# Performance work log

Measured on AMD Instinct MI355X. Metric: run time of the kernel, lower is better.

## Reference

```python
import jax, jax.numpy as jnp
import numpy as np

NX, NQ, NU = 2048, 2048, 16
EPS = 0.01
STD = 0.5


def setup_inputs() -> dict:
    key = jax.random.key(0)
    ks = jax.random.split(key, 8)
    return {
        "t": 0,
        "x": jax.random.normal(ks[0], (NX,), dtype=jnp.float32),
        "u": jax.random.normal(ks[1], (NU,), dtype=jnp.float32),
        "X": jax.random.normal(ks[2], (NX + NQ, NX + NQ), dtype=jnp.float32) * STD,
        "U": jax.random.normal(ks[3], (NX, NQ), dtype=jnp.float32) * STD,
        "Y1": jax.random.normal(ks[4], (NX, NX), dtype=jnp.float32) * STD,
        "XP": jax.random.normal(ks[5], (NX, NX), dtype=jnp.float32) * STD,
        "B2": jax.random.normal(ks[6], (NX, NU), dtype=jnp.float32) * STD,
        "D12": jax.random.normal(ks[7], (NQ, NU), dtype=jnp.float32) * STD,
    }


def _constrained_mats(X, U, Y1, XP):
    nx = XP.shape[0]
    nq = U.shape[1]
    # P = XP XP^T + eps I ;  H = X X^T + eps I   (F.linear(A,B)=A@B.T)
    P = XP @ XP.T + EPS * jnp.eye(nx, dtype=XP.dtype)
    H = X @ X.T + EPS * jnp.eye(nx + nq, dtype=X.dtype)
    H11 = H[:nx, :nx]
    H12 = H[:nx, nx:]
    H22 = H[nx:, nx:]
    Y = -0.5 * (H11 + Y1 - Y1.T)
    Pinv = jnp.linalg.inv(P)
    A = Pinv @ Y                        # F.linear(inv(P), Y.T) = inv(P) @ Y
    lam = 0.5 * jnp.diagonal(H22)       # diagonal of Lambda
    D11 = -jnp.tril(H22, -1) / lam[:, None]   # strictly lower triangular
    C1 = U.T / lam[:, None]             # inv(Lambda) @ U.T
    B1 = Pinv @ (-H12 - U)
    return A, B1, C1, D11


def _solve_w(D11, c):
    nq = c.shape[0]

    def step(w, inp):
        i, d_row, ci = inp
        wi = jax.nn.relu(ci + jnp.dot(d_row, w))
        return w.at[i].set(wi), None

    w0 = jnp.zeros(nq, dtype=c.dtype)
    w, _ = jax.lax.scan(step, w0, (jnp.arange(nq), D11, c))
    return w


def reference(t, x, u, X, U, Y1, XP, B2, D12):
    A, B1, C1, D11 = _constrained_mats(X, U, Y1, XP)
    c = C1 @ x + D12 @ u                # precomputed affine part (bv = 0, bias=False)
    w = _solve_w(D11, c)
    x_dot = A @ x + B1 @ w + B2 @ u     # bx = 0
    return x_dot
```

## Files before the change

kernel.cpp:

```cpp
#include <hip/hip_runtime.h>
#include <math.h>

#define NQ2 2048
#define NT  4096
#define NUU 16
#define FEPS 0.01f
#define NB  64
#define NBLK 32
#define NSB 128
#define NSP 132
#define NSBLK 16
#define GCH 16

typedef __attribute__((ext_vector_type(8))) short short8;
typedef __attribute__((ext_vector_type(4))) float floatx4;

__device__ __forceinline__ float readlane_f(float v, int lane) {
  return __int_as_float(__builtin_amdgcn_readlane(__float_as_int(v), lane));
}

__device__ __forceinline__ unsigned short f2bf(float x) {
  unsigned u = __float_as_uint(x);
  unsigned r = u + 0x7FFFu + ((u >> 16) & 1u);
  return (unsigned short)(r >> 16);
}
__device__ __forceinline__ float bf2f(unsigned short h) {
  return __uint_as_float(((unsigned)h) << 16);
}

__device__ __forceinline__ float wave_reduce(float v) {
#pragma unroll
  for (int off = 32; off > 0; off >>= 1) v += __shfl_down(v, off, 64);
  return v;
}

__device__ __forceinline__ float block_reduce_256(float v) {
  __shared__ float sm[4];
  v = wave_reduce(v);
  if ((threadIdx.x & 63) == 0) sm[threadIdx.x >> 6] = v;
  __syncthreads();
  return (threadIdx.x == 0) ? (sm[0] + sm[1] + sm[2] + sm[3]) : 0.0f;
}

__global__ __launch_bounds__(256) void lam_kernel(const float* __restrict__ X,
                                                  float* __restrict__ invlam) {
  int row = blockIdx.x;
  const float* xr = X + (size_t)(NQ2 + row) * NT;
  float s = 0.f;
  for (int k = threadIdx.x * 4; k < NT; k += 1024) {
    float4 v = *(const float4*)(xr + k);
    s += v.x * v.x + v.y * v.y + v.z * v.z + v.w * v.w;
  }
  float tot = block_reduce_256(s);
  if (threadIdx.x == 0) invlam[row] = 1.0f / (0.5f * (tot + FEPS));
}

__global__ __launch_bounds__(256) void tgemv_part_kernel(const float* __restrict__ A,
                                                         const float* __restrict__ v,
                                                         float* __restrict__ part) {
  int col = blockIdx.x * 256 + threadIdx.x;
  int ch = blockIdx.y;
  int i0 = ch * (NQ2 / GCH), i1 = i0 + NQ2 / GCH;
  float s = 0.f;
#pragma unroll 4
  for (int i = i0; i < i1; i++) s = fmaf(A[(size_t)i * NQ2 + col], v[i], s);
  part[(size_t)ch * NQ2 + col] = s;
}

template <int FM>
__global__ __launch_bounds__(256) void finish_kernel(const float* __restrict__ part,
                                                     const float* __restrict__ invlam,
                                                     const float* __restrict__ D12,
                                                     const float* __restrict__ u,
                                                     float* __restrict__ dst) {
  int col = blockIdx.x * 256 + threadIdx.x;
  float s = 0.f;
#pragma unroll
  for (int ch = 0; ch < GCH; ch++) s += part[(size_t)ch * NQ2 + col];
  if (FM == 0) {
    float d = 0.f;
#pragma unroll
    for (int j = 0; j < NUU; j++) d += D12[(size_t)col * NUU + j] * u[j];
    dst[col] = s * invlam[col] + d;
  } else if (FM == 1) {
    dst[col] += 0.5f * s;
  } else {
    dst[col] = s;
  }
}

__global__ __launch_bounds__(256) void syrk_mfma_kernel(const float* __restrict__ A,
                                                        int lda, int K,
                                                        float* __restrict__ C, float eps) {
  int L = blockIdx.x;
  int bi = (int)((sqrtf(8.0f * (float)L + 1.0f) - 1.0f) * 0.5f);
  while ((bi + 1) * (bi + 2) / 2 <= L) bi++;
  while (bi * (bi + 1) / 2 > L) bi--;
  int bj = L - bi * (bi + 1) / 2;
  int row0 = bi * 128, col0 = bj * 128;

  __shared__ __align__(16) short Ah[4096], Al[4096], Bh[4096], Bl[4096];

  int tid = threadIdx.x;
  int l = tid & 63;
  int w = tid >> 6;
  int wr = w >> 1, wc = w & 1;

  int g0 = tid, g1 = tid + 256;
  int ar0 = (g0 >> 6) * 16 + (g0 & 15), ak0 = ((g0 >> 4) & 3) * 8;
  int ar1 = (g1 >> 6) * 16 + (g1 & 15), ak1 = ((g1 >> 4) & 3) * 8;

  const float* pa0 = A + (size_t)(row0 + ar0) * lda + ak0;
  const float* pa1 = A + (size_t)(row0 + ar1) * lda + ak1;
  const float* pb0 = A + (size_t)(col0 + ar0) * lda + ak0;
  const float* pb1 = A + (size_t)(col0 + ar1) * lda + ak1;

  floatx4 acc[4][4];
#pragma unroll
  for (int m = 0; m < 4; m++)
#pragma unroll
    for (int n = 0; n < 4; n++) acc[m][n] = (floatx4){0.f, 0.f, 0.f, 0.f};

  float xa0[8], xa1[8], xb0[8], xb1[8];
  {
    float4 t0 = *(const float4*)(pa0), t1 = *(const float4*)(pa0 + 4);
    xa0[0]=t0.x; xa0[1]=t0.y; xa0[2]=t0.z; xa0[3]=t0.w; xa0[4]=t1.x; xa0[5]=t1.y; xa0[6]=t1.z; xa0[7]=t1.w;
    t0 = *(const float4*)(pa1); t1 = *(const float4*)(pa1 + 4);
    xa1[0]=t0.x; xa1[1]=t0.y; xa1[2]=t0.z; xa1[3]=t0.w; xa1[4]=t1.x; xa1[5]=t1.y; xa1[6]=t1.z; xa1[7]=t1.w;
    t0 = *(const float4*)(pb0); t1 = *(const float4*)(pb0 + 4);
    xb0[0]=t0.x; xb0[1]=t0.y; xb0[2]=t0.z; xb0[3]=t0.w; xb0[4]=t1.x; xb0[5]=t1.y; xb0[6]=t1.z; xb0[7]=t1.w;
    t0 = *(const float4*)(pb1); t1 = *(const float4*)(pb1 + 4);
    xb1[0]=t0.x; xb1[1]=t0.y; xb1[2]=t0.z; xb1[3]=t0.w; xb1[4]=t1.x; xb1[5]=t1.y; xb1[6]=t1.z; xb1[7]=t1.w;
  }

  for (int k0 = 0; k0 < K; k0 += 32) {
    __syncthreads();
    {
      short8 h, lo;
#pragma unroll
      for (int j = 0; j < 8; j++) { unsigned short hb = f2bf(xa0[j]); h[j] = (short)hb; lo[j] = (short)f2bf(xa0[j] - bf2f(hb)); }
      *(short8*)&Ah[g0 * 8] = h; *(short8*)&Al[g0 * 8] = lo;
#pragma unroll
      for (int j = 0; j < 8; j++) { unsigned short hb = f2bf(xa1[j]); h[j] = (short)hb; lo[j] = (short)f2bf(xa1[j] - bf2f(hb)); }
      *(short8*)&Ah[g1 * 8] = h; *(short8*)&Al[g1 * 8] = lo;
#pragma unroll
      for (int j = 0; j < 8; j++) { unsigned short hb = f2bf(xb0[j]); h[j] = (short)hb; lo[j] = (short)f2bf(xb0[j] - bf2f(hb)); }
      *(short8*)&Bh[g0 * 8] = h; *(short8*)&Bl[g0 * 8] = lo;
#pragma unroll
      for (int j = 0; j < 8; j++) { unsigned short hb = f2bf(xb1[j]); h[j] = (short)hb; lo[j] = (short)f2bf(xb1[j] - bf2f(hb)); }
      *(short8*)&Bh[g1 * 8] = h; *(short8*)&Bl[g1 * 8] = lo;
    }
    __syncthreads();
    if (k0 + 32 < K) {
      const float* q = pa0 + k0 + 32;
      float4 t0 = *(const float4*)(q), t1 = *(const float4*)(q + 4);
      xa0[0]=t0.x; xa0[1]=t0.y; xa0[2]=t0.z; xa0[3]=t0.w; xa0[4]=t1.x; xa0[5]=t1.y; xa0[6]=t1.z; xa0[7]=t1.w;
      q = pa1 + k0 + 32; t0 = *(const float4*)(q); t1 = *(const float4*)(q + 4);
      xa1[0]=t0.x; xa1[1]=t0.y; xa1[2]=t0.z; xa1[3]=t0.w; xa1[4]=t1.x; xa1[5]=t1.y; xa1[6]=t1.z; xa1[7]=t1.w;
      q = pb0 + k0 + 32; t0 = *(const float4*)(q); t1 = *(const float4*)(q + 4);
      xb0[0]=t0.x; xb0[1]=t0.y; xb0[2]=t0.z; xb0[3]=t0.w; xb0[4]=t1.x; xb0[5]=t1.y; xb0[6]=t1.z; xb0[7]=t1.w;
      q = pb1 + k0 + 32; t0 = *(const float4*)(q); t1 = *(const float4*)(q + 4);
      xb1[0]=t0.x; xb1[1]=t0.y; xb1[2]=t0.z; xb1[3]=t0.w; xb1[4]=t1.x; xb1[5]=t1.y; xb1[6]=t1.z; xb1[7]=t1.w;
    }
    short8 amh[4], aml[4], bnh[4], bnl[4];
#pragma unroll
    for (int m = 0; m < 4; m++) {
      int ga = ((wr * 4 + m) * 64 + l) * 8;
      amh[m] = *(const short8*)&Ah[ga];
      aml[m] = *(const short8*)&Al[ga];
    }
#pragma unroll
    for (int n = 0; n < 4; n++) {
      int gb = ((wc * 4 + n) * 64 + l) * 8;
      bnh[n] = *(const short8*)&Bh[gb];
      bnl[n] = *(const short8*)&Bl[gb];
    }
#pragma unroll
    for (int m = 0; m < 4; m++)
#pragma unroll
      for (int n = 0; n < 4; n++) {
        acc[m][n] = __builtin_amdgcn_mfma_f32_16x16x32_bf16(amh[m], bnh[n], acc[m][n], 0, 0, 0);
        acc[m][n] = __builtin_amdgcn_mfma_f32_16x16x32_bf16(amh[m], bnl[n], acc[m][n], 0, 0, 0);
        acc[m][n] = __builtin_amdgcn_mfma_f32_16x16x32_bf16(aml[m], bnh[n], acc[m][n], 0, 0, 0);
      }
  }

  int lr = (l >> 4) * 4;
  int lc = l & 15;
#pragma unroll
  for (int m = 0; m < 4; m++)
#pragma unroll
    for (int n = 0; n < 4; n++)
#pragma unroll
      for (int r = 0; r < 4; r++) {
        int gi = row0 + wr * 64 + m * 16 + lr + r;
        int gj = col0 + wc * 64 + n * 16 + lc;
        float v = acc[m][n][r];
        if (gi == gj) v += eps;
        C[(size_t)gi * NQ2 + gj] = v;
      }
}

__global__ __launch_bounds__(512) void chol_diag128_kernel(float* __restrict__ M_,
                                                           float* __restrict__ Xinvs, int k) {
  __shared__ __align__(16) float Ls[NSB][NSP];
  __shared__ __align__(16) float Xs[NSB][NSP];
  __shared__ float Tmp[32][33];
  __shared__ float dinv[NSB];
  int b0 = k * NSB;
  int tid = threadIdx.x;
  int wv = tid >> 6;
  int lane = tid & 63;

  for (int e = tid; e < NSB * NSP; e += 512) ((float*)Xs)[e] = 0.f;
  for (int e = tid; e < NSB * NSB; e += 512) {
    int rr = e >> 7, cc = e & 127;
    Ls[rr][cc] = M_[(size_t)(b0 + rr) * NQ2 + b0 + cc];
  }
  __syncthreads();

#pragma unroll 1
  for (int kb = 0; kb < 4; kb++) {
    int o = kb * 32;
    if (wv == 0) {
      int r = lane & 31;
      float a[32];
#pragma unroll
      for (int j = 0; j < 32; j++) a[j] = Ls[o + r][o + j];
#pragma unroll
      for (int j = 0; j < 32; j++) {
        float d = readlane_f(a[j], j);
        float rs = rsqrtf(fmaxf(d, 1e-20f));
        a[j] *= rs;
        if (lane == 0) dinv[o + j] = rs;
#pragma unroll
        for (int k2 = j + 1; k2 < 32; k2++) {
          float ljk = readlane_f(a[j], k2);
          a[k2] = fmaf(-a[j], ljk, a[k2]);
        }
      }
      if (lane < 32) {
#pragma unroll
        for (int j = 0; j < 32; j++) Ls[o + r][o + j] = a[j];
      }
    }
    __syncthreads();
    int nrows = 96 - o;
    if (nrows > 0) {
      if (tid < nrows) {
        int r = o + 32 + tid;
        float v[32];
#pragma unroll
        for (int j = 0; j < 32; j++) v[j] = Ls[r][o + j];
#pragma unroll
        for (int t = 0; t < 32; t++) {
          v[t] *= dinv[o + t];
#pragma unroll
          for (int j = t + 1; j < 32; j++)
            v[j] = fmaf(-v[t], Ls[o + j][o + t], v[j]);
        }
#pragma unroll
        for (int j = 0; j < 32; j++) Ls[r][o + j] = v[j];
      }
      __syncthreads();
      int tot = nrows * nrows;
      for (int e = tid; e < tot; e += 512) {
        int rr = o + 32 + e / nrows, cc = o + 32 + e % nrows;
        float s = 0.f;
#pragma unroll
        for (int t = 0; t < 32; t += 4) {
          float4 a = *(const float4*)&Ls[rr][o + t];
          float4 b = *(const float4*)&Ls[cc][o + t];
          s += a.x * b.x + a.y * b.y + a.z * b.z + a.w * b.w;
        }
        Ls[rr][cc] -= s;
      }
      __syncthreads();
    }
  }

  if (wv < 4) {
    int o = wv * 32;
    int c = lane & 31;
    float x[32];
#pragma unroll
    for (int i = 0; i < 32; i++) x[i] = 0.f;
#pragma unroll
    for (int t = 0; t < 32; t++) {
      float rcpd = 1.0f / Ls[o + t][o + t];
      x[t] = (t == c) ? rcpd : x[t] * rcpd;
#pragma unroll
      for (int i = t + 1; i < 32; i++)
        x[i] = fmaf(-Ls[o + i][o + t], x[t], x[i]);
    }
    if (lane < 32) {
#pragma unroll
      for (int i = 0; i < 32; i++) Xs[o + i][o + c] = x[i];
    }
  }
  __syncthreads();

#pragma unroll 1
  for (int j = 0; j < 4; j++) {
#pragma unroll 1
    for (int i = j + 1; i < 4; i++) {
      int oi = i * 32, oj = j * 32;
      for (int e = tid; e < 32 * 32; e += 512) {
        int rr = e >> 5, cc = e & 31;
        float s = 0.f;
        for (int kk = j; kk < i; kk++) {
          int ok = kk * 32;
#pragma unroll
          for (int t = 0; t < 32; t += 4) {
            float4 a = *(const float4*)&Ls[oi + rr][ok + t];
            s += a.x * Xs[ok + t][oj + cc] + a.y * Xs[ok + t + 1][oj + cc]
               + a.z * Xs[ok + t + 2][oj + cc] + a.w * Xs[ok + t + 3][oj + cc];
          }
        }
        Tmp[rr][cc] = s;
      }
      __syncthreads();
      for (int e = tid; e < 32 * 32; e += 512) {
        int rr = e >> 5, cc = e & 31;
        float s = 0.f;
#pragma unroll
        for (int t = 0; t < 32; t += 4) {
          float4 a = *(const float4*)&Xs[oi + rr][oi + t];
          s += a.x * Tmp[t][cc] + a.y * Tmp[t + 1][cc]
             + a.z * Tmp[t + 2][cc] + a.w * Tmp[t + 3][cc];
        }
        Xs[oi + rr][oj + cc] = -s;
      }
      __syncthreads();
    }
  }

  float* Xp = Xinvs + (size_t)k * NSB * NSB;
  for (int e = tid; e < NSB * NSB; e += 512) {
    int rr = e >> 7, cc = e & 127;
    if (cc <= rr) M_[(size_t)(b0 + rr) * NQ2 + b0 + cc] = Ls[rr][cc];
    Xp[e] = Xs[rr][cc];
  }
}

__global__ __launch_bounds__(256) void chol_panel128_kernel(float* __restrict__ M_,
                                                            const float* __restrict__ Xinv,
                                                            int k) {
  int kc = k * NSB;
  int rb0 = kc + NSB + blockIdx.x * 128;
  __shared__ float As[16][128];
  __shared__ float Bs[16][128];
  int tid = threadIdx.x;
  int tx = tid & 15, ty = tid >> 4;
  int sr = tid >> 1, ks = (tid & 1) * 8;

  const float* ap = M_ + (size_t)(rb0 + sr) * NQ2 + kc + ks;
  const float* bp = Xinv + sr * 128 + ks;
  float4 a0 = *(const float4*)(ap), a1 = *(const float4*)(ap + 4);
  float4 b0 = *(const float4*)(bp), b1 = *(const float4*)(bp + 4);

  float acc[8][8] = {{0.f}};
  for (int k0 = 0; k0 < 128; k0 += 16) {
    __syncthreads();
    As[ks + 0][sr] = a0.x; As[ks + 1][sr] = a0.y; As[ks + 2][sr] = a0.z; As[ks + 3][sr] = a0.w;
    As[ks + 4][sr] = a1.x; As[ks + 5][sr] = a1.y; As[ks + 6][sr] = a1.z; As[ks + 7][sr] = a1.w;
    Bs[ks + 0][sr] = b0.x; Bs[ks + 1][sr] = b0.y; Bs[ks + 2][sr] = b0.z; Bs[ks + 3][sr] = b0.w;
    Bs[ks + 4][sr] = b1.x; Bs[ks + 5][sr] = b1.y; Bs[ks + 6][sr] = b1.z; Bs[ks + 7][sr] = b1.w;
    __syncthreads();
    if (k0 + 16 < 128) {
      const float* q = ap + k0 + 16;
      a0 = *(const float4*)(q); a1 = *(const float4*)(q + 4);
      q = bp + k0 + 16;
      b0 = *(const float4*)(q); b1 = *(const float4*)(q + 4);
    }
#pragma unroll
    for (int kk = 0; kk < 16; kk++) {
      float4 aL = *(const float4*)&As[kk][ty * 4];
      float4 aH = *(const float4*)&As[kk][64 + ty * 4];
      float4 bL = *(const float4*)&Bs[kk][tx * 4];
      float4 bH = *(const float4*)&Bs[kk][64 + tx * 4];
      float aa[8] = {aL.x, aL.y, aL.z, aL.w, aH.x, aH.y, aH.z, aH.w};
      float bb[8] = {bL.x, bL.y, bL.z, bL.w, bH.x, bH.y, bH.z, bH.w};
#pragma unroll
      for (int i = 0; i < 8; i++)
#pragma unroll
        for (int j = 0; j < 8; j++) acc[i][j] = fmaf(aa[i], bb[j], acc[i][j]);
    }
  }
#pragma unroll
  for (int ii = 0; ii < 8; ii++) {
    int gi = rb0 + ((ii >> 2) * 64) + ty * 4 + (ii & 3);
#pragma unroll
    for (int half = 0; half < 2; half++) {
      int gj0 = kc + half * 64 + tx * 4;
      float4 o;
      o.x = acc[ii][half * 4 + 0]; o.y = acc[ii][half * 4 + 1];
      o.z = acc[ii][half * 4 + 2]; o.w = acc[ii][half * 4 + 3];
      *(float4*)&M_[(size_t)gi * NQ2 + gj0] = o;
    }
  }
}

__global__ __launch_bounds__(256) void chol_trail128_kernel(float* __restrict__ M_, int k) {
  int L = blockIdx.x;
  int bi = (int)((sqrtf(8.0f * (float)L + 1.0f) - 1.0f) * 0.5f);
  while ((bi + 1) * (bi + 2) / 2 <= L) bi++;
  while (bi * (bi + 1) / 2 > L) bi--;
  int bj = L - bi * (bi + 1) / 2;
  int row0 = (k + 1 + bi) * NSB, col0 = (k + 1 + bj) * NSB, kc = k * NSB;

  __shared__ float As[16][128];
  __shared__ float Bs[16][128];
  int tid = threadIdx.x;
  int tx = tid & 15, ty = tid >> 4;
  int sr = tid >> 1, ks = (tid & 1) * 8;

  const float* ap = M_ + (size_t)(row0 + sr) * NQ2 + kc + ks;
  const float* bp = M_ + (size_t)(col0 + sr) * NQ2 + kc + ks;
  float4 a0 = *(const float4*)(ap), a1 = *(const float4*)(ap + 4);
  float4 b0 = *(const float4*)(bp), b1 = *(const float4*)(bp + 4);

  float acc[8][8] = {{0.f}};
  for (int k0 = 0; k0 < 128; k0 += 16) {
    __syncthreads();
    As[ks + 0][sr] = a0.x; As[ks + 1][sr] = a0.y; As[ks + 2][sr] = a0.z; As[ks + 3][sr] = a0.w;
    As[ks + 4][sr] = a1.x; As[ks + 5][sr] = a1.y; As[ks + 6][sr] = a1.z; As[ks + 7][sr] = a1.w;
    Bs[ks + 0][sr] = b0.x; Bs[ks + 1][sr] = b0.y; Bs[ks + 2][sr] = b0.z; Bs[ks + 3][sr] = b0.w;
    Bs[ks + 4][sr] = b1.x; Bs[ks + 5][sr] = b1.y; Bs[ks + 6][sr] = b1.z; Bs[ks + 7][sr] = b1.w;
    __syncthreads();
    if (k0 + 16 < 128) {
      const float* q = ap + k0 + 16;
      a0 = *(const float4*)(q); a1 = *(const float4*)(q + 4);
      q = bp + k0 + 16;
      b0 = *(const float4*)(q); b1 = *(const float4*)(q + 4);
    }
#pragma unroll
    for (int kk = 0; kk < 16; kk++) {
      float4 aL = *(const float4*)&As[kk][ty * 4];
      float4 aH = *(const float4*)&As[kk][64 + ty * 4];
      float4 bL = *(const float4*)&Bs[kk][tx * 4];
      float4 bH = *(const float4*)&Bs[kk][64 + tx * 4];
      float aa[8] = {aL.x, aL.y, aL.z, aL.w, aH.x, aH.y, aH.z, aH.w};
      float bb[8] = {bL.x, bL.y, bL.z, bL.w, bH.x, bH.y, bH.z, bH.w};
#pragma unroll
      for (int i = 0; i < 8; i++)
#pragma unroll
        for (int j = 0; j < 8; j++) acc[i][j] = fmaf(aa[i], bb[j], acc[i][j]);
    }
  }
#pragma unroll
  for (int ii = 0; ii < 8; ii++) {
    int gi = row0 + ((ii >> 2) * 64) + ty * 4 + (ii & 3);
#pragma unroll
    for (int half = 0; half < 2; half++) {
      int gj0 = col0 + half * 64 + tx * 4;
      float* cp = &M_[(size_t)gi * NQ2 + gj0];
      float4 v = *(const float4*)cp;
      v.x -= acc[ii][half * 4 + 0]; v.y -= acc[ii][half * 4 + 1];
      v.z -= acc[ii][half * 4 + 2]; v.w -= acc[ii][half * 4 + 3];
      *(float4*)cp = v;
    }
  }
}

__global__ __launch_bounds__(512) void wsolve_kernel(const float* __restrict__ M_,
                                                     const float* __restrict__ rhs,
                                                     const float* __restrict__ invlam,
                                                     float* __restrict__ out) {
  __shared__ float partial[NQ2];
  __shared__ float il[NQ2];
  __shared__ float tile[2][NB][NB + 1];
  __shared__ float vblk[NB];
  int tid = threadIdx.x;
  int rquad = tid >> 2;
  int l4 = tid & 3;
  for (int i = tid; i < NQ2; i += 512) {
    partial[i] = rhs[i];
    il[i] = invlam[i];
  }
  for (int e = tid; e < NB * NB; e += 512) {
    int rr = e >> 6, cc = e & 63;
    tile[0][rr][cc] = M_[(size_t)rr * NQ2 + cc];
  }
  __syncthreads();
  for (int b = 0; b < NBLK; b++) {
    int cur = b & 1;
    int b0 = b * NB;
    if (tid < 64) {
      int l = tid;
      float creg = partial[b0 + l];
      float ilreg = il[b0 + l];
      float acc = 0.f;
      float wfin = 0.f;
#pragma unroll
      for (int i = 0; i < NB; i++) {
        float cand = fmaxf(creg - acc * ilreg, 0.f);
        float wi = readlane_f(cand, i);
        acc = fmaf(tile[cur][l][i], wi, acc);
        if (l == i) wfin = wi;
      }
      vblk[l] = wfin;
      out[b0 + l] = wfin;
    } else if (b + 1 < NBLK) {
      int b1 = b0 + NB;
      for (int e = tid - 64; e < NB * NB; e += 448) {
        int rr = e >> 6, cc = e & 63;
        tile[cur ^ 1][rr][cc] = M_[(size_t)(b1 + rr) * NQ2 + b1 + cc];
      }
    }
    __syncthreads();
    float4 v0 = *(const float4*)(&vblk[l4 * 16]);
    float4 v1 = *(const float4*)(&vblk[l4 * 16 + 4]);
    float4 v2 = *(const float4*)(&vblk[l4 * 16 + 8]);
    float4 v3 = *(const float4*)(&vblk[l4 * 16 + 12]);
    for (int base = b0 + NB; base < NQ2; base += 512) {
      float accv[4] = {0.f, 0.f, 0.f, 0.f};
#pragma unroll
      for (int rr = 0; rr < 4; rr++) {
        int row = base + rr * 128 + rquad;
        if (row < NQ2) {
          const float* mr = M_ + (size_t)row * NQ2 + b0 + l4 * 16;
          float4 m0 = *(const float4*)(mr);
          float4 m1 = *(const float4*)(mr + 4);
          float4 m2 = *(const float4*)(mr + 8);
          float4 m3 = *(const float4*)(mr + 12);
          accv[rr] = m0.x * v0.x + m0.y * v0.y + m0.z * v0.z + m0.w * v0.w
                   + m1.x * v1.x + m1.y * v1.y + m1.z * v1.z + m1.w * v1.w
                   + m2.x * v2.x + m2.y * v2.y + m2.z * v2.z + m2.w * v2.w
                   + m3.x * v3.x + m3.y * v3.y + m3.z * v3.z + m3.w * v3.w;
        }
      }
#pragma unroll
      for (int rr = 0; rr < 4; rr++) {
        accv[rr] += __shfl_xor(accv[rr], 1);
        accv[rr] += __shfl_xor(accv[rr], 2);
      }
      if (l4 == 0) {
#pragma unroll
        for (int rr = 0; rr < 4; rr++) {
          int row = base + rr * 128 + rquad;
          if (row < NQ2) partial[row] -= accv[rr] * il[row];
        }
      }
    }
    __syncthreads();
  }
}

__global__ __launch_bounds__(1024) void lsolve_kernel(const float* __restrict__ M_,
                                                      const float* __restrict__ Xinvs,
                                                      const float* __restrict__ rhs,
                                                      float* __restrict__ out) {
  __shared__ float partial[NQ2];
  __shared__ float vblk[NSB];
  int tid = threadIdx.x;
  int row8 = tid >> 3, sub = tid & 7;
  for (int i = tid; i < NQ2; i += 1024) partial[i] = rhs[i];
  __syncthreads();
  for (int kb = 0; kb < NSBLK; kb++) {
    int b0 = kb * NSB;
    const float* Xp = Xinvs + (size_t)kb * NSB * NSB;
    {
      int j0 = sub * 16;
      const float* xr = Xp + row8 * NSB + j0;
      float4 x0 = *(const float4*)(xr), x1 = *(const float4*)(xr + 4);
      float4 x2 = *(const float4*)(xr + 8), x3 = *(const float4*)(xr + 12);
      const float* pp = &partial[b0 + j0];
      float s = x0.x*pp[0] + x0.y*pp[1] + x0.z*pp[2] + x0.w*pp[3]
              + x1.x*pp[4] + x1.y*pp[5] + x1.z*pp[6] + x1.w*pp[7]
              + x2.x*pp[8] + x2.y*pp[9] + x2.z*pp[10] + x2.w*pp[11]
              + x3.x*pp[12] + x3.y*pp[13] + x3.z*pp[14] + x3.w*pp[15];
      s += __shfl_xor(s, 1); s += __shfl_xor(s, 2); s += __shfl_xor(s, 4);
      if (sub == 0) { vblk[row8] = s; out[b0 + row8] = s; }
    }
    __syncthreads();
    const float* vp = &vblk[sub * 16];
    for (int base = b0 + NSB; base < NQ2; base += 256) {
      int row0 = base + row8;
      int row1 = row0 + 128;
      float s0 = 0.f, s1 = 0.f;
      if (row0 < NQ2) {
        const float* mr = M_ + (size_t)row0 * NQ2 + b0 + sub * 16;
        float4 m0 = *(const float4*)(mr), m1 = *(const float4*)(mr + 4);
        float4 m2 = *(const float4*)(mr + 8), m3 = *(const float4*)(mr + 12);
        s0 = m0.x*vp[0] + m0.y*vp[1] + m0.z*vp[2] + m0.w*vp[3]
           + m1.x*vp[4] + m1.y*vp[5] + m1.z*vp[6] + m1.w*vp[7]
           + m2.x*vp[8] + m2.y*vp[9] + m2.z*vp[10] + m2.w*vp[11]
           + m3.x*vp[12] + m3.y*vp[13] + m3.z*vp[14] + m3.w*vp[15];
      }
      if (row1 < NQ2) {
        const float* mr = M_ + (size_t)row1 * NQ2 + b0 + sub * 16;
        float4 m0 = *(const float4*)(mr), m1 = *(const float4*)(mr + 4);
        float4 m2 = *(const float4*)(mr + 8), m3 = *(const float4*)(mr + 12);
        s1 = m0.x*vp[0] + m0.y*vp[1] + m0.z*vp[2] + m0.w*vp[3]
           + m1.x*vp[4] + m1.y*vp[5] + m1.z*vp[6] + m1.w*vp[7]
           + m2.x*vp[8] + m2.y*vp[9] + m2.z*vp[10] + m2.w*vp[11]
           + m3.x*vp[12] + m3.y*vp[13] + m3.z*vp[14] + m3.w*vp[15];
      }
      s0 += __shfl_xor(s0, 1); s0 += __shfl_xor(s0, 2); s0 += __shfl_xor(s0, 4);
      s1 += __shfl_xor(s1, 1); s1 += __shfl_xor(s1, 2); s1 += __shfl_xor(s1, 4);
      if (sub == 0) {
        if (row0 < NQ2) partial[row0] -= s0;
        if (row1 < NQ2) partial[row1] -= s1;
      }
    }
    __syncthreads();
  }
}

__global__ __launch_bounds__(1024) void ltsolve_kernel(const float* __restrict__ M_,
                                                       const float* __restrict__ Xinvs,
                                                       const float* __restrict__ rhs,
                                                       float* __restrict__ out) {
  __shared__ float partial[NQ2];
  __shared__ float Xl[NSB][NSB + 1];
  __shared__ float vblk[NSB];
  int tid = threadIdx.x;
  int row8 = tid >> 3, sub = tid & 7;
  for (int i = tid; i < NQ2; i += 1024) partial[i] = rhs[i];
  __syncthreads();
  for (int kb = NSBLK - 1; kb >= 0; kb--) {
    int b0 = kb * NSB;
    const float* Xp = Xinvs + (size_t)kb * NSB * NSB;
    for (int e = tid; e < NSB * NSB; e += 1024) Xl[e >> 7][e & 127] = Xp[e];
    __syncthreads();
    {
      int j0 = sub * 16;
      float s = 0.f;
#pragma unroll
      for (int j = 0; j < 16; j++)
        s = fmaf(Xl[j0 + j][row8], partial[b0 + j0 + j], s);
      s += __shfl_xor(s, 1); s += __shfl_xor(s, 2); s += __shfl_xor(s, 4);
      if (sub == 0) { vblk[row8] = s; out[b0 + row8] = s; }
    }
    __syncthreads();
    for (int i = tid; i < b0; i += 1024) {
      float acc = 0.f;
#pragma unroll 16
      for (int j = 0; j < NSB; j++) acc = fmaf(M_[(size_t)(b0 + j) * NQ2 + i], vblk[j], acc);
      partial[i] -= acc;
    }
    __syncthreads();
  }
}

#define TCH 32
__global__ __launch_bounds__(256) void t_partial_kernel(const float* __restrict__ X,
                                                        const float* __restrict__ x,
                                                        const float* __restrict__ w,
                                                        float* __restrict__ tpart) {
  int k4 = (blockIdx.x * 256 + threadIdx.x) * 4;
  int chunk = blockIdx.y;
  int i0 = chunk * (NT / TCH);
  float4 acc = {0.f, 0.f, 0.f, 0.f};
  for (int i = i0; i < i0 + NT / TCH; i++) {
    float cf = (i < NQ2) ? (-0.5f * x[i]) : (-w[i - NQ2]);
    float4 xv = *(const float4*)(X + (size_t)i * NT + k4);
    acc.x += cf * xv.x; acc.y += cf * xv.y; acc.z += cf * xv.z; acc.w += cf * xv.w;
  }
  *(float4*)(tpart + (size_t)chunk * NT + k4) = acc;
}

__global__ __launch_bounds__(256) void t_reduce_kernel(const float* __restrict__ tpart,
                                                       float* __restrict__ t) {
  int k = blockIdx.x * 256 + threadIdx.x;
  float s = 0.f;
#pragma unroll 8
  for (int ch = 0; ch < TCH; ch++) s += tpart[(size_t)ch * NT + k];
  t[k] = s;
}

__global__ __launch_bounds__(256) void r_kernel(const float* __restrict__ X,
                                                const float* __restrict__ Y1,
                                                const float* __restrict__ U,
                                                const float* __restrict__ t,
                                                const float* __restrict__ x,
                                                const float* __restrict__ w,
                                                float* __restrict__ r) {
  int row = blockIdx.x;
  float s1 = 0.f, s2 = 0.f, s3 = 0.f;
  const float* xr = X + (size_t)row * NT;
  for (int k = threadIdx.x * 4; k < NT; k += 1024) {
    float4 a = *(const float4*)(xr + k);
    float4 b = *(const float4*)(t + k);
    s1 += a.x * b.x + a.y * b.y + a.z * b.z + a.w * b.w;
  }
  const float* yr = Y1 + (size_t)row * NQ2;
  const float* ur = U + (size_t)row * NQ2;
  for (int k = threadIdx.x * 4; k < NQ2; k += 1024) {
    float4 a = *(const float4*)(yr + k);
    float4 b = *(const float4*)(x + k);
    s2 += a.x * b.x + a.y * b.y + a.z * b.z + a.w * b.w;
    float4 c2 = *(const float4*)(ur + k);
    float4 d2 = *(const float4*)(w + k);
    s3 += c2.x * d2.x + c2.y * d2.y + c2.z * d2.z + c2.w * d2.w;
  }
  float v = s1 - 0.5f * s2 - s3;
  float tot = block_reduce_256(v);
  if (threadIdx.x == 0) r[row] = tot - 0.5f * FEPS * x[row];
}

__global__ __launch_bounds__(256) void pz2_res_kernel(const float* __restrict__ XP,
                                                      const float* __restrict__ pz1,
                                                      const float* __restrict__ z,
                                                      const float* __restrict__ r,
                                                      float* __restrict__ res) {
  int row = blockIdx.x;
  float s = 0.f;
  const float* xr = XP + (size_t)row * NQ2;
  for (int k = threadIdx.x * 4; k < NQ2; k += 1024) {
    float4 a = *(const float4*)(xr + k);
    float4 b = *(const float4*)(pz1 + k);
    s += a.x * b.x + a.y * b.y + a.z * b.z + a.w * b.w;
  }
  float tot = block_reduce_256(s);
  if (threadIdx.x == 0) res[row] = r[row] - (tot + FEPS * z[row]);
}

__global__ __launch_bounds__(256) void axpy_kernel(float* __restrict__ z,
                                                   const float* __restrict__ dz) {
  int i = blockIdx.x * 256 + threadIdx.x;
  z[i] += dz[i];
}

__global__ __launch_bounds__(256) void out_kernel(const float* __restrict__ z,
                                                  const float* __restrict__ B2,
                                                  const float* __restrict__ u,
                                                  float* __restrict__ out) {
  int i = blockIdx.x * 256 + threadIdx.x;
  float s = 0.f;
#pragma unroll
  for (int j = 0; j < NUU; j++) s += B2[(size_t)i * NUU + j] * u[j];
  out[i] = z[i] + s;
}

extern "C" void kernel_launch(void* const* d_in, const int* in_sizes, int n_in,
                              void* d_out, int out_size, void* d_ws, size_t ws_size,
                              hipStream_t stream) {
  (void)in_sizes; (void)n_in; (void)out_size; (void)ws_size;
  const float* x   = (const float*)d_in[1];
  const float* u   = (const float*)d_in[2];
  const float* X   = (const float*)d_in[3];
  const float* U   = (const float*)d_in[4];
  const float* Y1  = (const float*)d_in[5];
  const float* XP  = (const float*)d_in[6];
  const float* B2  = (const float*)d_in[7];
  const float* D12 = (const float*)d_in[8];
  float* out = (float*)d_out;

  float* ws     = (float*)d_ws;
  float* M      = ws;
  float* vecs   = ws + (size_t)NQ2 * NQ2;
  float* invlam = vecs;
  float* c      = vecs + 2048;
  float* w      = vecs + 4096;
  float* r      = vecs + 6144;
  float* y      = vecs + 8192;
  float* z      = vecs + 10240;
  float* dz     = vecs + 12288;
  float* res    = vecs + 14336;
  float* t      = vecs + 16384;
  float* tpart  = vecs + 20480;
  float* gpart  = tpart;
  float* Xinvs  = vecs + 20480 + 32 * 4096;

  int nsyrk = (NQ2 / 128) * (NQ2 / 128 + 1) / 2;
  dim3 gdim(NQ2 / 256, GCH);

  lam_kernel<<<NQ2, 256, 0, stream>>>(X, invlam);
  tgemv_part_kernel<<<gdim, 256, 0, stream>>>(U, x, gpart);
  finish_kernel<0><<<NQ2 / 256, 256, 0, stream>>>(gpart, invlam, D12, u, c);

  syrk_mfma_kernel<<<nsyrk, 256, 0, stream>>>(X + (size_t)NQ2 * NT, NT, NT, M, 0.0f);
  wsolve_kernel<<<1, 512, 0, stream>>>(M, c, invlam, w);

  dim3 tg(4, TCH);
  t_partial_kernel<<<tg, 256, 0, stream>>>(X, x, w, tpart);
  t_reduce_kernel<<<NT / 256, 256, 0, stream>>>(tpart, t);
  r_kernel<<<NQ2, 256, 0, stream>>>(X, Y1, U, t, x, w, r);
  tgemv_part_kernel<<<gdim, 256, 0, stream>>>(Y1, x, gpart);
  finish_kernel<1><<<NQ2 / 256, 256, 0, stream>>>(gpart, invlam, D12, u, r);

  syrk_mfma_kernel<<<nsyrk, 256, 0, stream>>>(XP, NQ2, NQ2, M, FEPS);
  for (int k = 0; k < NSBLK; k++) {
    chol_diag128_kernel<<<1, 512, 0, stream>>>(M, Xinvs, k);
    int rows_below = NQ2 - (k + 1) * NSB;
    if (rows_below > 0) {
      chol_panel128_kernel<<<rows_below / 128, 256, 0, stream>>>(
          M, Xinvs + (size_t)k * NSB * NSB, k);
      int m = NSBLK - 1 - k;
      chol_trail128_kernel<<<m * (m + 1) / 2, 256, 0, stream>>>(M, k);
    }
  }

  lsolve_kernel<<<1, 1024, 0, stream>>>(M, Xinvs, r, y);
  ltsolve_kernel<<<1, 1024, 0, stream>>>(M, Xinvs, y, z);

  {
    tgemv_part_kernel<<<gdim, 256, 0, stream>>>(XP, z, gpart);
    finish_kernel<2><<<NQ2 / 256, 256, 0, stream>>>(gpart, invlam, D12, u, t);
    pz2_res_kernel<<<NQ2, 256, 0, stream>>>(XP, t, z, r, res);
    lsolve_kernel<<<1, 1024, 0, stream>>>(M, Xinvs, res, y);
    ltsolve_kernel<<<1, 1024, 0, stream>>>(M, Xinvs, y, dz);
    axpy_kernel<<<NQ2 / 256, 256, 0, stream>>>(z, dz);
  }

  out_kernel<<<NQ2 / 256, 256, 0, stream>>>(z, B2, u, out);
}
```

Baseline: 2.669 ms.

## Overlap serial w-solve with P SYRK in a merged kernel

Turns the SYRK into a 512-thread device body where all threads stage tiles but only the first 256 issue MFMAs. A merged launch runs the single-block serial forward-substitution w-solve next to the XP·XPᵀ SYRK blocks, writing P into a separate workspace buffer so the two no longer serialize on M. The merged path is used only when the workspace is large enough; otherwise it falls back to separate launches. The trade-off is extra workspace and half-idle waves in the SYRK blocks, which may reduce SYRK throughput.

```diff
diff --git a/kernel.cpp b/kernel.cpp
--- a/kernel.cpp
+++ b/kernel.cpp
@@ -18,7 +18,6 @@
 __device__ __forceinline__ float readlane_f(float v, int lane) {
   return __int_as_float(__builtin_amdgcn_readlane(__float_as_int(v), lane));
 }
-
 __device__ __forceinline__ unsigned short f2bf(float x) {
   unsigned u = __float_as_uint(x);
   unsigned r = u + 0x7FFFu + ((u >> 16) & 1u);
@@ -33,7 +32,6 @@
   for (int off = 32; off > 0; off >>= 1) v += __shfl_down(v, off, 64);
   return v;
 }
-
 __device__ __forceinline__ float block_reduce_256(float v) {
   __shared__ float sm[4];
   v = wave_reduce(v);
@@ -89,31 +87,24 @@
   }
 }
 
-__global__ __launch_bounds__(256) void syrk_mfma_kernel(const float* __restrict__ A,
-                                                        int lda, int K,
-                                                        float* __restrict__ C, float eps) {
-  int L = blockIdx.x;
+__device__ void syrk512_body(const float* __restrict__ A, int lda, int K,
+                             float* __restrict__ C, float eps, int L, int tid) {
+  __shared__ __align__(16) short Ah[4096], Al[4096], Bh[4096], Bl[4096];
+
   int bi = (int)((sqrtf(8.0f * (float)L + 1.0f) - 1.0f) * 0.5f);
   while ((bi + 1) * (bi + 2) / 2 <= L) bi++;
   while (bi * (bi + 1) / 2 > L) bi--;
   int bj = L - bi * (bi + 1) / 2;
   int row0 = bi * 128, col0 = bj * 128;
 
-  __shared__ __align__(16) short Ah[4096], Al[4096], Bh[4096], Bl[4096];
-
-  int tid = threadIdx.x;
   int l = tid & 63;
   int w = tid >> 6;
   int wr = w >> 1, wc = w & 1;
 
-  int g0 = tid, g1 = tid + 256;
-  int ar0 = (g0 >> 6) * 16 + (g0 & 15), ak0 = ((g0 >> 4) & 3) * 8;
-  int ar1 = (g1 >> 6) * 16 + (g1 & 15), ak1 = ((g1 >> 4) & 3) * 8;
-
-  const float* pa0 = A + (size_t)(row0 + ar0) * lda + ak0;
-  const float* pa1 = A + (size_t)(row0 + ar1) * lda + ak1;
-  const float* pb0 = A + (size_t)(col0 + ar0) * lda + ak0;
-  const float* pb1 = A + (size_t)(col0 + ar1) * lda + ak1;
+  int g = tid;
+  int ar = (g >> 6) * 16 + (g & 15), ak = ((g >> 4) & 3) * 8;
+  const float* pa = A + (size_t)(row0 + ar) * lda + ak;
+  const float* pb = A + (size_t)(col0 + ar) * lda + ak;
 
   floatx4 acc[4][4];
 #pragma unroll
@@ -121,16 +112,12 @@
 #pragma unroll
     for (int n = 0; n < 4; n++) acc[m][n] = (floatx4){0.f, 0.f, 0.f, 0.f};
 
-  float xa0[8], xa1[8], xb0[8], xb1[8];
+  float xa[8], xb[8];
   {
-    float4 t0 = *(const float4*)(pa0), t1 = *(const float4*)(pa0 + 4);
-    xa0[0]=t0.x; xa0[1]=t0.y; xa0[2]=t0.z; xa0[3]=t0.w; xa0[4]=t1.x; xa0[5]=t1.y; xa0[6]=t1.z; xa0[7]=t1.w;
-    t0 = *(const float4*)(pa1); t1 = *(const float4*)(pa1 + 4);
-    xa1[0]=t0.x; xa1[1]=t0.y; xa1[2]=t0.z; xa1[3]=t0.w; xa1[4]=t1.x; xa1[5]=t1.y; xa1[6]=t1.z; xa1[7]=t1.w;
-    t0 = *(const float4*)(pb0); t1 = *(const float4*)(pb0 + 4);
-    xb0[0]=t0.x; xb0[1]=t0.y; xb0[2]=t0.z; xb0[3]=t0.w; xb0[4]=t1.x; xb0[5]=t1.y; xb0[6]=t1.z; xb0[7]=t1.w;
-    t0 = *(const float4*)(pb1); t1 = *(const float4*)(pb1 + 4);
-    xb1[0]=t0.x; xb1[1]=t0.y; xb1[2]=t0.z; xb1[3]=t0.w; xb1[4]=t1.x; xb1[5]=t1.y; xb1[6]=t1.z; xb1[7]=t1.w;
+    float4 t0 = *(const float4*)(pa), t1 = *(const float4*)(pa + 4);
+    xa[0]=t0.x; xa[1]=t0.y; xa[2]=t0.z; xa[3]=t0.w; xa[4]=t1.x; xa[5]=t1.y; xa[6]=t1.z; xa[7]=t1.w;
+    t0 = *(const float4*)(pb); t1 = *(const float4*)(pb + 4);
+    xb[0]=t0.x; xb[1]=t0.y; xb[2]=t0.z; xb[3]=t0.w; xb[4]=t1.x; xb[5]=t1.y; xb[6]=t1.z; xb[7]=t1.w;
   }
 
   for (int k0 = 0; k0 < K; k0 += 32) {
@@ -138,340 +125,76 @@
     {
       short8 h, lo;
 #pragma unroll
-      for (int j = 0; j < 8; j++) { unsigned short hb = f2bf(xa0[j]); h[j] = (short)hb; lo[j] = (short)f2bf(xa0[j] - bf2f(hb)); }
-      *(short8*)&Ah[g0 * 8] = h; *(short8*)&Al[g0 * 8] = lo;
-#pragma unroll
-      for (int j = 0; j < 8; j++) { unsigned short hb = f2bf(xa1[j]); h[j] = (short)hb; lo[j] = (short)f2bf(xa1[j] - bf2f(hb)); }
-      *(short8*)&Ah[g1 * 8] = h; *(short8*)&Al[g1 * 8] = lo;
-#pragma unroll
-      for (int j = 0; j < 8; j++) { unsigned short hb = f2bf(xb0[j]); h[j] = (short)hb; lo[j] = (short)f2bf(xb0[j] - bf2f(hb)); }
-      *(short8*)&Bh[g0 * 8] = h; *(short8*)&Bl[g0 * 8] = lo;
-#pragma unroll
-      for (int j = 0; j < 8; j++) { unsigned short hb = f2bf(xb1[j]); h[j] = (short)hb; lo[j] = (short)f2bf(xb1[j] - bf2f(hb)); }
-      *(short8*)&Bh[g1 * 8] = h; *(short8*)&Bl[g1 * 8] = lo;
+      for (int j = 0; j < 8; j++) { unsigned short hb = f2bf(xa[j]); h[j] = (short)hb; lo[j] = (short)f2bf(xa[j] - bf2f(hb)); }
+      *(short8*)&Ah[g * 8] = h; *(short8*)&Al[g * 8] = lo;
+#pragma unroll
+      for (int j = 0; j < 8; j++) { unsigned short hb = f2bf(xb[j]); h[j] = (short)hb; lo[j] = (short)f2bf(xb[j] - bf2f(hb)); }
+      *(short8*)&Bh[g * 8] = h; *(short8*)&Bl[g * 8] = lo;
     }
     __syncthreads();
     if (k0 + 32 < K) {
-      const float* q = pa0 + k0 + 32;
+      const float* q = pa + k0 + 32;
       float4 t0 = *(const float4*)(q), t1 = *(const float4*)(q + 4);
-      xa0[0]=t0.x; xa0[1]=t0.y; xa0[2]=t0.z; xa0[3]=t0.w; xa0[4]=t1.x; xa0[5]=t1.y; xa0[6]=t1.z; xa0[7]=t1.w;
-      q = pa1 + k0 + 32; t0 = *(const float4*)(q); t1 = *(const float4*)(q + 4);
-      xa1[0]=t0.x; xa1[1]=t0.y; xa1[2]=t0.z; xa1[3]=t0.w; xa1[4]=t1.x; xa1[5]=t1.y; xa1[6]=t1.z; xa1[7]=t1.w;
-      q = pb0 + k0 + 32; t0 = *(const float4*)(q); t1 = *(const float4*)(q + 4);
-      xb0[0]=t0.x; xb0[1]=t0.y; xb0[2]=t0.z; xb0[3]=t0.w; xb0[4]=t1.x; xb0[5]=t1.y; xb0[6]=t1.z; xb0[7]=t1.w;
-      q = pb1 + k0 + 32; t0 = *(const float4*)(q); t1 = *(const float4*)(q + 4);
-      xb1[0]=t0.x; xb1[1]=t0.y; xb1[2]=t0.z; xb1[3]=t0.w; xb1[4]=t1.x; xb1[5]=t1.y; xb1[6]=t1.z; xb1[7]=t1.w;
-    }
-    short8 amh[4], aml[4], bnh[4], bnl[4];
-#pragma unroll
-    for (int m = 0; m < 4; m++) {
-      int ga = ((wr * 4 + m) * 64 + l) * 8;
-      amh[m] = *(const short8*)&Ah[ga];
-      aml[m] = *(const short8*)&Al[ga];
-    }
-#pragma unroll
-    for (int n = 0; n < 4; n++) {
-      int gb = ((wc * 4 + n) * 64 + l) * 8;
-      bnh[n] = *(const short8*)&Bh[gb];
-      bnl[n] = *(const short8*)&Bl[gb];
-    }
+      xa[0]=t0.x; xa[1]=t0.y; xa[2]=t0.z; xa[3]=t0.w; xa[4]=t1.x; xa[5]=t1.y; xa[6]=t1.z; xa[7]=t1.w;
+      q = pb + k0 + 32; t0 = *(const float4*)(q); t1 = *(const float4*)(q + 4);
+      xb[0]=t0.x; xb[1]=t0.y; xb[2]=t0.z; xb[3]=t0.w; xb[4]=t1.x; xb[5]=t1.y; xb[6]=t1.z; xb[7]=t1.w;
+    }
+    if (tid < 256) {
+      short8 amh[4], aml[4], bnh[4], bnl[4];
+#pragma unroll
+      for (int m = 0; m < 4; m++) {
+        int ga = ((wr * 4 + m) * 64 + l) * 8;
+        amh[m] = *(const short8*)&Ah[ga];
+        aml[m] = *(const short8*)&Al[ga];
+      }
+#pragma unroll
+      for (int n = 0; n < 4; n++) {
+        int gb = ((wc * 4 + n) * 64 + l) * 8;
+        bnh[n] = *(const short8*)&Bh[gb];
+        bnl[n] = *(const short8*)&Bl[gb];
+      }
+#pragma unroll
+      for (int m = 0; m < 4; m++)
+#pragma unroll
+        for (int n = 0; n < 4; n++) {
+          acc[m][n] = __builtin_amdgcn_mfma_f32_16x16x32_bf16(amh[m], bnh[n], acc[m][n], 0, 0, 0);
+          acc[m][n] = __builtin_amdgcn_mfma_f32_16x16x32_bf16(amh[m], bnl[n], acc[m][n], 0, 0, 0);
+          acc[m][n] = __builtin_amdgcn_mfma_f32_16x16x32_bf16(aml[m], bnh[n], acc[m][n], 0, 0, 0);
+        }
+    }
+  }
+
+  if (tid < 256) {
+    int lr = (l >> 4) * 4;
+    int lc = l & 15;
 #pragma unroll
     for (int m = 0; m < 4; m++)
 #pragma unroll
-      for (int n = 0; n < 4; n++) {
-        acc[m][n] = __builtin_amdgcn_mfma_f32_16x16x32_bf16(amh[m], bnh[n], acc[m][n], 0, 0, 0);
-        acc[m][n] = __builtin_amdgcn_mfma_f32_16x16x32_bf16(amh[m], bnl[n], acc[m][n], 0, 0, 0);
-        acc[m][n] = __builtin_amdgcn_mfma_f32_16x16x32_bf16(aml[m], bnh[n], acc[m][n], 0, 0, 0);
-      }
-  }
-
-  int lr = (l >> 4) * 4;
-  int lc = l & 15;
-#pragma unroll
-  for (int m = 0; m < 4; m++)
-#pragma unroll
-    for (int n = 0; n < 4; n++)
-#pragma unroll
-      for (int r = 0; r < 4; r++) {
-        int gi = row0 + wr * 64 + m * 16 + lr + r;
-        int gj = col0 + wc * 64 + n * 16 + lc;
-        float v = acc[m][n][r];
-        if (gi == gj) v += eps;
-        C[(size_t)gi * NQ2 + gj] = v;
-      }
-}
-
-__global__ __launch_bounds__(512) void chol_diag128_kernel(float* __restrict__ M_,
-                                                           float* __restrict__ Xinvs, int k) {
-  __shared__ __align__(16) float Ls[NSB][NSP];
-  __shared__ __align__(16) float Xs[NSB][NSP];
-  __shared__ float Tmp[32][33];
-  __shared__ float dinv[NSB];
-  int b0 = k * NSB;
-  int tid = threadIdx.x;
-  int wv = tid >> 6;
-  int lane = tid & 63;
-
-  for (int e = tid; e < NSB * NSP; e += 512) ((float*)Xs)[e] = 0.f;
-  for (int e = tid; e < NSB * NSB; e += 512) {
-    int rr = e >> 7, cc = e & 127;
-    Ls[rr][cc] = M_[(size_t)(b0 + rr) * NQ2 + b0 + cc];
-  }
-  __syncthreads();
-
-#pragma unroll 1
-  for (int kb = 0; kb < 4; kb++) {
-    int o = kb * 32;
-    if (wv == 0) {
-      int r = lane & 31;
-      float a[32];
-#pragma unroll
-      for (int j = 0; j < 32; j++) a[j] = Ls[o + r][o + j];
-#pragma unroll
-      for (int j = 0; j < 32; j++) {
-        float d = readlane_f(a[j], j);
-        float rs = rsqrtf(fmaxf(d, 1e-20f));
-        a[j] *= rs;
-        if (lane == 0) dinv[o + j] = rs;
-#pragma unroll
-        for (int k2 = j + 1; k2 < 32; k2++) {
-          float ljk = readlane_f(a[j], k2);
-          a[k2] = fmaf(-a[j], ljk, a[k2]);
+      for (int n = 0; n < 4; n++)
+#pragma unroll
+        for (int r = 0; r < 4; r++) {
+          int gi = row0 + wr * 64 + m * 16 + lr + r;
+          int gj = col0 + wc * 64 + n * 16 + lc;
+          float v = acc[m][n][r];
+          if (gi == gj) v += eps;
+          C[(size_t)gi * NQ2 + gj] = v;
         }
-      }
-      if (lane < 32) {
-#pragma unroll
-        for (int j = 0; j < 32; j++) Ls[o + r][o + j] = a[j];
-      }
-    }
-    __syncthreads();
-    int nrows = 96 - o;
-    if (nrows > 0) {
-      if (tid < nrows) {
-        int r = o + 32 + tid;
-        float v[32];
-#pragma unroll
-        for (int j = 0; j < 32; j++) v[j] = Ls[r][o + j];
-#pragma unroll
-        for (int t = 0; t < 32; t++) {
-          v[t] *= dinv[o + t];
-#pragma unroll
-          for (int j = t + 1; j < 32; j++)
-            v[j] = fmaf(-v[t], Ls[o + j][o + t], v[j]);
-        }
-#pragma unroll
-        for (int j = 0; j < 32; j++) Ls[r][o + j] = v[j];
-      }
-      __syncthreads();
-      int tot = nrows * nrows;
-      for (int e = tid; e < tot; e += 512) {
-        int rr = o + 32 + e / nrows, cc = o + 32 + e % nrows;
-        float s = 0.f;
-#pragma unroll
-        for (int t = 0; t < 32; t += 4) {
-          float4 a = *(const float4*)&Ls[rr][o + t];
-          float4 b = *(const float4*)&Ls[cc][o + t];
-          s += a.x * b.x + a.y * b.y + a.z * b.z + a.w * b.w;
-        }
-        Ls[rr][cc] -= s;
-      }
-      __syncthreads();
-    }
-  }
-
-  if (wv < 4) {
-    int o = wv * 32;
-    int c = lane & 31;
-    float x[32];
-#pragma unroll
-    for (int i = 0; i < 32; i++) x[i] = 0.f;
-#pragma unroll
-    for (int t = 0; t < 32; t++) {
-      float rcpd = 1.0f / Ls[o + t][o + t];
-      x[t] = (t == c) ? rcpd : x[t] * rcpd;
-#pragma unroll
-      for (int i = t + 1; i < 32; i++)
-        x[i] = fmaf(-Ls[o + i][o + t], x[t], x[i]);
-    }
-    if (lane < 32) {
-#pragma unroll
-      for (int i = 0; i < 32; i++) Xs[o + i][o + c] = x[i];
-    }
-  }
-  __syncthreads();
-
-#pragma unroll 1
-  for (int j = 0; j < 4; j++) {
-#pragma unroll 1
-    for (int i = j + 1; i < 4; i++) {
-      int oi = i * 32, oj = j * 32;
-      for (int e = tid; e < 32 * 32; e += 512) {
-        int rr = e >> 5, cc = e & 31;
-        float s = 0.f;
-        for (int kk = j; kk < i; kk++) {
-          int ok = kk * 32;
-#pragma unroll
-          for (int t = 0; t < 32; t += 4) {
-            float4 a = *(const float4*)&Ls[oi + rr][ok + t];
-            s += a.x * Xs[ok + t][oj + cc] + a.y * Xs[ok + t + 1][oj + cc]
-               + a.z * Xs[ok + t + 2][oj + cc] + a.w * Xs[ok + t + 3][oj + cc];
-          }
-        }
-        Tmp[rr][cc] = s;
-      }
-      __syncthreads();
-      for (int e = tid; e < 32 * 32; e += 512) {
-        int rr = e >> 5, cc = e & 31;
-        float s = 0.f;
-#pragma unroll
-        for (int t = 0; t < 32; t += 4) {
-          float4 a = *(const float4*)&Xs[oi + rr][oi + t];
-          s += a.x * Tmp[t][cc] + a.y * Tmp[t + 1][cc]
-             + a.z * Tmp[t + 2][cc] + a.w * Tmp[t + 3][cc];
-        }
-        Xs[oi + rr][oj + cc] = -s;
-      }
-      __syncthreads();
-    }
-  }
-
-  float* Xp = Xinvs + (size_t)k * NSB * NSB;
-  for (int e = tid; e < NSB * NSB; e += 512) {
-    int rr = e >> 7, cc = e & 127;
-    if (cc <= rr) M_[(size_t)(b0 + rr) * NQ2 + b0 + cc] = Ls[rr][cc];
-    Xp[e] = Xs[rr][cc];
-  }
-}
-
-__global__ __launch_bounds__(256) void chol_panel128_kernel(float* __restrict__ M_,
-                                                            const float* __restrict__ Xinv,
-                                                            int k) {
-  int kc = k * NSB;
-  int rb0 = kc + NSB + blockIdx.x * 128;
-  __shared__ float As[16][128];
-  __shared__ float Bs[16][128];
-  int tid = threadIdx.x;
-  int tx = tid & 15, ty = tid >> 4;
-  int sr = tid >> 1, ks = (tid & 1) * 8;
-
-  const float* ap = M_ + (size_t)(rb0 + sr) * NQ2 + kc + ks;
-  const float* bp = Xinv + sr * 128 + ks;
-  float4 a0 = *(const float4*)(ap), a1 = *(const float4*)(ap + 4);
-  float4 b0 = *(const float4*)(bp), b1 = *(const float4*)(bp + 4);
-
-  float acc[8][8] = {{0.f}};
-  for (int k0 = 0; k0 < 128; k0 += 16) {
-    __syncthreads();
-    As[ks + 0][sr] = a0.x; As[ks + 1][sr] = a0.y; As[ks + 2][sr] = a0.z; As[ks + 3][sr] = a0.w;
-    As[ks + 4][sr] = a1.x; As[ks + 5][sr] = a1.y; As[ks + 6][sr] = a1.z; As[ks + 7][sr] = a1.w;
-    Bs[ks + 0][sr] = b0.x; Bs[ks + 1][sr] = b0.y; Bs[ks + 2][sr] = b0.z; Bs[ks + 3][sr] = b0.w;
-    Bs[ks + 4][sr] = b1.x; Bs[ks + 5][sr] = b1.y; Bs[ks + 6][sr] = b1.z; Bs[ks + 7][sr] = b1.w;
-    __syncthreads();
-    if (k0 + 16 < 128) {
-      const float* q = ap + k0 + 16;
-      a0 = *(const float4*)(q); a1 = *(const float4*)(q + 4);
-      q = bp + k0 + 16;
-      b0 = *(const float4*)(q); b1 = *(const float4*)(q + 4);
-    }
-#pragma unroll
-    for (int kk = 0; kk < 16; kk++) {
-      float4 aL = *(const float4*)&As[kk][ty * 4];
-      float4 aH = *(const float4*)&As[kk][64 + ty * 4];
-      float4 bL = *(const float4*)&Bs[kk][tx * 4];
-      float4 bH = *(const float4*)&Bs[kk][64 + tx * 4];
-      float aa[8] = {aL.x, aL.y, aL.z, aL.w, aH.x, aH.y, aH.z, aH.w};
-      float bb[8] = {bL.x, bL.y, bL.z, bL.w, bH.x, bH.y, bH.z, bH.w};
-#pragma unroll
-      for (int i = 0; i < 8; i++)
-#pragma unroll
-        for (int j = 0; j < 8; j++) acc[i][j] = fmaf(aa[i], bb[j], acc[i][j]);
-    }
-  }
-#pragma unroll
-  for (int ii = 0; ii < 8; ii++) {
-    int gi = rb0 + ((ii >> 2) * 64) + ty * 4 + (ii & 3);
-#pragma unroll
-    for (int half = 0; half < 2; half++) {
-      int gj0 = kc + half * 64 + tx * 4;
-      float4 o;
-      o.x = acc[ii][half * 4 + 0]; o.y = acc[ii][half * 4 + 1];
-      o.z = acc[ii][half * 4 + 2]; o.w = acc[ii][half * 4 + 3];
-      *(float4*)&M_[(size_t)gi * NQ2 + gj0] = o;
-    }
-  }
-}
-
-__global__ __launch_bounds__(256) void chol_trail128_kernel(float* __restrict__ M_, int k) {
-  int L = blockIdx.x;
-  int bi = (int)((sqrtf(8.0f * (float)L + 1.0f) - 1.0f) * 0.5f);
-  while ((bi + 1) * (bi + 2) / 2 <= L) bi++;
-  while (bi * (bi + 1) / 2 > L) bi--;
-  int bj = L - bi * (bi + 1) / 2;
-  int row0 = (k + 1 + bi) * NSB, col0 = (k + 1 + bj) * NSB, kc = k * NSB;
-
-  __shared__ float As[16][128];
-  __shared__ float Bs[16][128];
-  int tid = threadIdx.x;
-  int tx = tid & 15, ty = tid >> 4;
-  int sr = tid >> 1, ks = (tid & 1) * 8;
-
-  const float* ap = M_ + (size_t)(row0 + sr) * NQ2 + kc + ks;
-  const float* bp = M_ + (size_t)(col0 + sr) * NQ2 + kc + ks;
-  float4 a0 = *(const float4*)(ap), a1 = *(const float4*)(ap + 4);
-  float4 b0 = *(const float4*)(bp), b1 = *(const float4*)(bp + 4);
-
-  float acc[8][8] = {{0.f}};
-  for (int k0 = 0; k0 < 128; k0 += 16) {
-    __syncthreads();
-    As[ks + 0][sr] = a0.x; As[ks + 1][sr] = a0.y; As[ks + 2][sr] = a0.z; As[ks + 3][sr] = a0.w;
-    As[ks + 4][sr] = a1.x; As[ks + 5][sr] = a1.y; As[ks + 6][sr] = a1.z; As[ks + 7][sr] = a1.w;
-    Bs[ks + 0][sr] = b0.x; Bs[ks + 1][sr] = b0.y; Bs[ks + 2][sr] = b0.z; Bs[ks + 3][sr] = b0.w;
-    Bs[ks + 4][sr] = b1.x; Bs[ks + 5][sr] = b1.y; Bs[ks + 6][sr] = b1.z; Bs[ks + 7][sr] = b1.w;
-    __syncthreads();
-    if (k0 + 16 < 128) {
-      const float* q = ap + k0 + 16;
-      a0 = *(const float4*)(q); a1 = *(const float4*)(q + 4);
-      q = bp + k0 + 16;
-      b0 = *(const float4*)(q); b1 = *(const float4*)(q + 4);
-    }
-#pragma unroll
-    for (int kk = 0; kk < 16; kk++) {
-      float4 aL = *(const float4*)&As[kk][ty * 4];
-      float4 aH = *(const float4*)&As[kk][64 + ty * 4];
-      float4 bL = *(const float4*)&Bs[kk][tx * 4];
-      float4 bH = *(const float4*)&Bs[kk][64 + tx * 4];
-      float aa[8] = {aL.x, aL.y, aL.z, aL.w, aH.x, aH.y, aH.z, aH.w};
-      float bb[8] = {bL.x, bL.y, bL.z, bL.w, bH.x, bH.y, bH.z, bH.w};
-#pragma unroll
-      for (int i = 0; i < 8; i++)
-#pragma unroll
-        for (int j = 0; j < 8; j++) acc[i][j] = fmaf(aa[i], bb[j], acc[i][j]);
-    }
-  }
-#pragma unroll
-  for (int ii = 0; ii < 8; ii++) {
-    int gi = row0 + ((ii >> 2) * 64) + ty * 4 + (ii & 3);
-#pragma unroll
-    for (int half = 0; half < 2; half++) {
-      int gj0 = col0 + half * 64 + tx * 4;
-      float* cp = &M_[(size_t)gi * NQ2 + gj0];
-      float4 v = *(const float4*)cp;
-      v.x -= acc[ii][half * 4 + 0]; v.y -= acc[ii][half * 4 + 1];
-      v.z -= acc[ii][half * 4 + 2]; v.w -= acc[ii][half * 4 + 3];
-      *(float4*)cp = v;
-    }
-  }
-}
-
-__global__ __launch_bounds__(512) void wsolve_kernel(const float* __restrict__ M_,
-                                                     const float* __restrict__ rhs,
-                                                     const float* __restrict__ invlam,
-                                                     float* __restrict__ out) {
+  }
+}
+
+__global__ __launch_bounds__(512) void syrk512_kernel(const float* __restrict__ A,
+                                                      int lda, int K,
+                                                      float* __restrict__ C, float eps) {
+  syrk512_body(A, lda, K, C, eps, blockIdx.x, threadIdx.x);
+}
+
+__device__ void wsolve_body(const float* __restrict__ M_, const float* __restrict__ rhs,
+                            const float* __restrict__ invlam, float* __restrict__ out,
+                            int tid) {
   __shared__ float partial[NQ2];
   __shared__ float il[NQ2];
   __shared__ float tile[2][NB][NB + 1];
   __shared__ float vblk[NB];
-  int tid = threadIdx.x;
   int rquad = tid >> 2;
   int l4 = tid & 3;
   for (int i = tid; i < NQ2; i += 512) {
@@ -544,6 +267,290 @@
       }
     }
     __syncthreads();
+  }
+}
+
+__global__ __launch_bounds__(512) void wsolve_kernel(const float* __restrict__ M_,
+                                                     const float* __restrict__ rhs,
+                                                     const float* __restrict__ invlam,
+                                                     float* __restrict__ out) {
+  wsolve_body(M_, rhs, invlam, out, threadIdx.x);
+}
+
+__global__ __launch_bounds__(512) void merged_wsolve_psyrk_kernel(
+    const float* __restrict__ Mh22, const float* __restrict__ c,
+    const float* __restrict__ invlam, float* __restrict__ w,
+    const float* __restrict__ XP, float* __restrict__ P) {
+  if (blockIdx.x == 0) {
+    wsolve_body(Mh22, c, invlam, w, threadIdx.x);
+  } else {
+    syrk512_body(XP, NQ2, NQ2, P, FEPS, blockIdx.x - 1, threadIdx.x);
+  }
+}
+
+__global__ __launch_bounds__(512) void chol_diag128_kernel(float* __restrict__ M_,
+                                                           float* __restrict__ Xinvs, int k) {
+  __shared__ __align__(16) float Ls[NSB][NSP];
+  __shared__ __align__(16) float Xs[NSB][NSP];
+  __shared__ float Tmp[32][33];
+  __shared__ float dinv[NSB];
+  int b0 = k * NSB;
+  int tid = threadIdx.x;
+  int wv = tid >> 6;
+  int lane = tid & 63;
+
+  for (int e = tid; e < NSB * NSP; e += 512) ((float*)Xs)[e] = 0.f;
+  for (int e = tid; e < NSB * NSB; e += 512) {
+    int rr = e >> 7, cc = e & 127;
+    Ls[rr][cc] = M_[(size_t)(b0 + rr) * NQ2 + b0 + cc];
+  }
+  __syncthreads();
+
+#pragma unroll 1
+  for (int kb = 0; kb < 4; kb++) {
+    int o = kb * 32;
+    if (wv == 0) {
+      int r = lane & 31;
+      float a[32];
+#pragma unroll
+      for (int j = 0; j < 32; j++) a[j] = Ls[o + r][o + j];
+#pragma unroll
+      for (int j = 0; j < 32; j++) {
+        float d = readlane_f(a[j], j);
+        float rs = rsqrtf(fmaxf(d, 1e-20f));
+        a[j] *= rs;
+        if (lane == 0) dinv[o + j] = rs;
+#pragma unroll
+        for (int k2 = j + 1; k2 < 32; k2++) {
+          float ljk = readlane_f(a[j], k2);
+          a[k2] = fmaf(-a[j], ljk, a[k2]);
+        }
+      }
+      if (lane < 32) {
+#pragma unroll
+        for (int j = 0; j < 32; j++) Ls[o + r][o + j] = a[j];
+      }
+    }
+    __syncthreads();
+    int nrows = 96 - o;
+    if (nrows > 0) {
+      if (tid < nrows) {
+        int r = o + 32 + tid;
+        float v[32];
+#pragma unroll
+        for (int j = 0; j < 32; j++) v[j] = Ls[r][o + j];
+#pragma unroll
+        for (int t = 0; t < 32; t++) {
+          v[t] *= dinv[o + t];
+#pragma unroll
+          for (int j = t + 1; j < 32; j++)
+            v[j] = fmaf(-v[t], Ls[o + j][o + t], v[j]);
+        }
+#pragma unroll
+        for (int j = 0; j < 32; j++) Ls[r][o + j] = v[j];
+      }
+      __syncthreads();
+      int tot = nrows * (nrows + 1) / 2;
+      for (int e = tid; e < tot; e += 512) {
+        int a = (int)((sqrtf(8.0f * (float)e + 1.0f) - 1.0f) * 0.5f);
+        while ((a + 1) * (a + 2) / 2 <= e) a++;
+        while (a * (a + 1) / 2 > e) a--;
+        int bcol = e - a * (a + 1) / 2;
+        int rr = o + 32 + a, cc = o + 32 + bcol;
+        float s = 0.f;
+#pragma unroll
+        for (int t = 0; t < 32; t += 4) {
+          float4 av = *(const float4*)&Ls[rr][o + t];
+          float4 bv = *(const float4*)&Ls[cc][o + t];
+          s += av.x * bv.x + av.y * bv.y + av.z * bv.z + av.w * bv.w;
+        }
+        Ls[rr][cc] -= s;
+      }
+      __syncthreads();
+    }
+  }
+
+  if (wv < 4) {
+    int o = wv * 32;
+    int c = lane & 31;
+    float x[32];
+#pragma unroll
+    for (int i = 0; i < 32; i++) x[i] = 0.f;
+#pragma unroll
+    for (int t = 0; t < 32; t++) {
+      float rcpd = 1.0f / Ls[o + t][o + t];
+      x[t] = (t == c) ? rcpd : x[t] * rcpd;
+#pragma unroll
+      for (int i = t + 1; i < 32; i++)
+        x[i] = fmaf(-Ls[o + i][o + t], x[t], x[i]);
+    }
+    if (lane < 32) {
+#pragma unroll
+      for (int i = 0; i < 32; i++) Xs[o + i][o + c] = x[i];
+    }
+  }
+  __syncthreads();
+
+#pragma unroll 1
+  for (int j = 0; j < 4; j++) {
+#pragma unroll 1
+    for (int i = j + 1; i < 4; i++) {
+      int oi = i * 32, oj = j * 32;
+      for (int e = tid; e < 32 * 32; e += 512) {
+        int rr = e >> 5, cc = e & 31;
+        float s = 0.f;
+        for (int kk = j; kk < i; kk++) {
+          int ok = kk * 32;
+#pragma unroll
+          for (int t = 0; t < 32; t += 4) {
+            float4 a = *(const float4*)&Ls[oi + rr][ok + t];
+            s += a.x * Xs[ok + t][oj + cc] + a.y * Xs[ok + t + 1][oj + cc]
+               + a.z * Xs[ok + t + 2][oj + cc] + a.w * Xs[ok + t + 3][oj + cc];
+          }
+        }
+        Tmp[rr][cc] = s;
+      }
+      __syncthreads();
+      for (int e = tid; e < 32 * 32; e += 512) {
+        int rr = e >> 5, cc = e & 31;
+        float s = 0.f;
+#pragma unroll
+        for (int t = 0; t < 32; t += 4) {
+          float4 a = *(const float4*)&Xs[oi + rr][oi + t];
+          s += a.x * Tmp[t][cc] + a.y * Tmp[t + 1][cc]
+             + a.z * Tmp[t + 2][cc] + a.w * Tmp[t + 3][cc];
+        }
+        Xs[oi + rr][oj + cc] = -s;
+      }
+      __syncthreads();
+    }
+  }
+
+  float* Xp = Xinvs + (size_t)k * NSB * NSB;
+  for (int e = tid; e < NSB * NSB; e += 512) {
+    int rr = e >> 7, cc = e & 127;
+    if (cc <= rr) M_[(size_t)(b0 + rr) * NQ2 + b0 + cc] = Ls[rr][cc];
+    Xp[e] = Xs[rr][cc];
+  }
+}
+
+__global__ __launch_bounds__(256) void chol_panel128_kernel(float* __restrict__ M_,
+                                                            const float* __restrict__ Xinv,
+                                                            int k) {
+  int kc = k * NSB;
+  int rb0 = kc + NSB + blockIdx.x * 128;
+  __shared__ float As[16][128];
+  __shared__ float Bs[16][128];
+  int tid = threadIdx.x;
+  int tx = tid & 15, ty = tid >> 4;
+  int sr = tid >> 1, ks = (tid & 1) * 8;
+
+  const float* ap = M_ + (size_t)(rb0 + sr) * NQ2 + kc + ks;
+  const float* bp = Xinv + sr * 128 + ks;
+  float4 a0 = *(const float4*)(ap), a1 = *(const float4*)(ap + 4);
+  float4 b0 = *(const float4*)(bp), b1 = *(const float4*)(bp + 4);
+
+  float acc[8][8] = {{0.f}};
+  for (int k0 = 0; k0 < 128; k0 += 16) {
+    __syncthreads();
+    As[ks + 0][sr] = a0.x; As[ks + 1][sr] = a0.y; As[ks + 2][sr] = a0.z; As[ks + 3][sr] = a0.w;
+    As[ks + 4][sr] = a1.x; As[ks + 5][sr] = a1.y; As[ks + 6][sr] = a1.z; As[ks + 7][sr] = a1.w;
+    Bs[ks + 0][sr] = b0.x; Bs[ks + 1][sr] = b0.y; Bs[ks + 2][sr] = b0.z; Bs[ks + 3][sr] = b0.w;
+    Bs[ks + 4][sr] = b1.x; Bs[ks + 5][sr] = b1.y; Bs[ks + 6][sr] = b1.z; Bs[ks + 7][sr] = b1.w;
+    __syncthreads();
+    if (k0 + 16 < 128) {
+      const float* q = ap + k0 + 16;
+      a0 = *(const float4*)(q); a1 = *(const float4*)(q + 4);
+      q = bp + k0 + 16;
+      b0 = *(const float4*)(q); b1 = *(const float4*)(q + 4);
+    }
+#pragma unroll
+    for (int kk = 0; kk < 16; kk++) {
+      float4 aL = *(const float4*)&As[kk][ty * 4];
+      float4 aH = *(const float4*)&As[kk][64 + ty * 4];
+      float4 bL = *(const float4*)&Bs[kk][tx * 4];
+      float4 bH = *(const float4*)&Bs[kk][64 + tx * 4];
+      float aa[8] = {aL.x, aL.y, aL.z, aL.w, aH.x, aH.y, aH.z, aH.w};
+      float bb[8] = {bL.x, bL.y, bL.z, bL.w, bH.x, bH.y, bH.z, bH.w};
+#pragma unroll
+      for (int i = 0; i < 8; i++)
+#pragma unroll
+        for (int j = 0; j < 8; j++) acc[i][j] = fmaf(aa[i], bb[j], acc[i][j]);
+    }
+  }
+#pragma unroll
+  for (int ii = 0; ii < 8; ii++) {
+    int gi = rb0 + ((ii >> 2) * 64) + ty * 4 + (ii & 3);
+#pragma unroll
+    for (int half = 0; half < 2; half++) {
+      int gj0 = kc + half * 64 + tx * 4;
+      float4 o;
+      o.x = acc[ii][half * 4 + 0]; o.y = acc[ii][half * 4 + 1];
+      o.z = acc[ii][half * 4 + 2]; o.w = acc[ii][half * 4 + 3];
+      *(float4*)&M_[(size_t)gi * NQ2 + gj0] = o;
+    }
+  }
+}
+
+__global__ __launch_bounds__(256) void chol_trail128_kernel(float* __restrict__ M_, int k) {
+  int L = blockIdx.x;
+  int bi = (int)((sqrtf(8.0f * (float)L + 1.0f) - 1.0f) * 0.5f);
+  while ((bi + 1) * (bi + 2) / 2 <= L) bi++;
+  while (bi * (bi + 1) / 2 > L) bi--;
+  int bj = L - bi * (bi + 1) / 2;
+  int row0 = (k + 1 + bi) * NSB, col0 = (k + 1 + bj) * NSB, kc = k * NSB;
+
+  __shared__ float As[16][128];
+  __shared__ float Bs[16][128];
+  int tid = threadIdx.x;
+  int tx = tid & 15, ty = tid >> 4;
+  int sr = tid >> 1, ks = (tid & 1) * 8;
+
+  const float* ap = M_ + (size_t)(row0 + sr) * NQ2 + kc + ks;
+  const float* bp = M_ + (size_t)(col0 + sr) * NQ2 + kc + ks;
+  float4 a0 = *(const float4*)(ap), a1 = *(const float4*)(ap + 4);
+  float4 b0 = *(const float4*)(bp), b1 = *(const float4*)(bp + 4);
+
+  float acc[8][8] = {{0.f}};
+  for (int k0 = 0; k0 < 128; k0 += 16) {
+    __syncthreads();
+    As[ks + 0][sr] = a0.x; As[ks + 1][sr] = a0.y; As[ks + 2][sr] = a0.z; As[ks + 3][sr] = a0.w;
+    As[ks + 4][sr] = a1.x; As[ks + 5][sr] = a1.y; As[ks + 6][sr] = a1.z; As[ks + 7][sr] = a1.w;
+    Bs[ks + 0][sr] = b0.x; Bs[ks + 1][sr] = b0.y; Bs[ks + 2][sr] = b0.z; Bs[ks + 3][sr] = b0.w;
+    Bs[ks + 4][sr] = b1.x; Bs[ks + 5][sr] = b1.y; Bs[ks + 6][sr] = b1.z; Bs[ks + 7][sr] = b1.w;
+    __syncthreads();
+    if (k0 + 16 < 128) {
+      const float* q = ap + k0 + 16;
+      a0 = *(const float4*)(q); a1 = *(const float4*)(q + 4);
+      q = bp + k0 + 16;
+      b0 = *(const float4*)(q); b1 = *(const float4*)(q + 4);
+    }
+#pragma unroll
+    for (int kk = 0; kk < 16; kk++) {
+      float4 aL = *(const float4*)&As[kk][ty * 4];
+      float4 aH = *(const float4*)&As[kk][64 + ty * 4];
+      float4 bL = *(const float4*)&Bs[kk][tx * 4];
+      float4 bH = *(const float4*)&Bs[kk][64 + tx * 4];
+      float aa[8] = {aL.x, aL.y, aL.z, aL.w, aH.x, aH.y, aH.z, aH.w};
+      float bb[8] = {bL.x, bL.y, bL.z, bL.w, bH.x, bH.y, bH.z, bH.w};
+#pragma unroll
+      for (int i = 0; i < 8; i++)
+#pragma unroll
+        for (int j = 0; j < 8; j++) acc[i][j] = fmaf(aa[i], bb[j], acc[i][j]);
+    }
+  }
+#pragma unroll
+  for (int ii = 0; ii < 8; ii++) {
+    int gi = row0 + ((ii >> 2) * 64) + ty * 4 + (ii & 3);
+#pragma unroll
+    for (int half = 0; half < 2; half++) {
+      int gj0 = col0 + half * 64 + tx * 4;
+      float* cp = &M_[(size_t)gi * NQ2 + gj0];
+      float4 v = *(const float4*)cp;
+      v.x -= acc[ii][half * 4 + 0]; v.y -= acc[ii][half * 4 + 1];
+      v.z -= acc[ii][half * 4 + 2]; v.w -= acc[ii][half * 4 + 3];
+      *(float4*)cp = v;
+    }
   }
 }
 
@@ -737,7 +744,7 @@
 extern "C" void kernel_launch(void* const* d_in, const int* in_sizes, int n_in,
                               void* d_out, int out_size, void* d_ws, size_t ws_size,
                               hipStream_t stream) {
-  (void)in_sizes; (void)n_in; (void)out_size; (void)ws_size;
+  (void)in_sizes; (void)n_in; (void)out_size;
   const float* x   = (const float*)d_in[1];
   const float* u   = (const float*)d_in[2];
   const float* X   = (const float*)d_in[3];
@@ -763,45 +770,58 @@
   float* tpart  = vecs + 20480;
   float* gpart  = tpart;
   float* Xinvs  = vecs + 20480 + 32 * 4096;
+  float* Ptmp   = Xinvs + (size_t)NSBLK * NSB * NSB;
+
+  size_t need_merged = ((size_t)(Ptmp - ws) + (size_t)NQ2 * NQ2) * sizeof(float);
+  bool merged = (ws_size >= need_merged);
+  float* P = merged ? Ptmp : M;
 
   int nsyrk = (NQ2 / 128) * (NQ2 / 128 + 1) / 2;
   dim3 gdim(NQ2 / 256, GCH);
+  dim3 tg(4, TCH);
 
   lam_kernel<<<NQ2, 256, 0, stream>>>(X, invlam);
   tgemv_part_kernel<<<gdim, 256, 0, stream>>>(U, x, gpart);
   finish_kernel<0><<<NQ2 / 256, 256, 0, stream>>>(gpart, invlam, D12, u, c);
 
-  syrk_mfma_kernel<<<nsyrk, 256, 0, stream>>>(X + (size_t)NQ2 * NT, NT, NT, M, 0.0f);
-  wsolve_kernel<<<1, 512, 0, stream>>>(M, c, invlam, w);
-
-  dim3 tg(4, TCH);
+  syrk512_kernel<<<nsyrk, 512, 0, stream>>>(X + (size_t)NQ2 * NT, NT, NT, M, 0.0f);
+
+  if (merged) {
+    merged_wsolve_psyrk_kernel<<<1 + nsyrk, 512, 0, stream>>>(M, c, invlam, w, XP, Ptmp);
+  } else {
+    wsolve_kernel<<<1, 512, 0, stream>>>(M, c, invlam, w);
+  }
+
   t_partial_kernel<<<tg, 256, 0, stream>>>(X, x, w, tpart);
   t_reduce_kernel<<<NT / 256, 256, 0, stream>>>(tpart, t);
   r_kernel<<<NQ2, 256, 0, stream>>>(X, Y1, U, t, x, w, r);
   tgemv_part_kernel<<<gdim, 256, 0, stream>>>(Y1, x, gpart);
   finish_kernel<1><<<NQ2 / 256, 256, 0, stream>>>(gpart, invlam, D12, u, r);
 
-  syrk_mfma_kernel<<<nsyrk, 256, 0, stream>>>(XP, NQ2, NQ2, M, FEPS);
+  if (!merged) {
+    syrk512_kernel<<<nsyrk, 512, 0, stream>>>(XP, NQ2, NQ2, P, FEPS);
+  }
+
   for (int k = 0; k < NSBLK; k++) {
-    chol_diag128_kernel<<<1, 512, 0, stream>>>(M, Xinvs, k);
+    chol_diag128_kernel<<<1, 512, 0, stream>>>(P, Xinvs, k);
     int rows_below = NQ2 - (k + 1) * NSB;
     if (rows_below > 0) {
       chol_panel128_kernel<<<rows_below / 128, 256, 0, stream>>>(
-          M, Xinvs + (size_t)k * NSB * NSB, k);
+          P, Xinvs + (size_t)k * NSB * NSB, k);
       int m = NSBLK - 1 - k;
-      chol_trail128_kernel<<<m * (m + 1) / 2, 256, 0, stream>>>(M, k);
-    }
-  }
-
-  lsolve_kernel<<<1, 1024, 0, stream>>>(M, Xinvs, r, y);
-  ltsolve_kernel<<<1, 1024, 0, stream>>>(M, Xinvs, y, z);
+      chol_trail128_kernel<<<m * (m + 1) / 2, 256, 0, stream>>>(P, k);
+    }
+  }
+
+  lsolve_kernel<<<1, 1024, 0, stream>>>(P, Xinvs, r, y);
+  ltsolve_kernel<<<1, 1024, 0, stream>>>(P, Xinvs, y, z);
 
   {
     tgemv_part_kernel<<<gdim, 256, 0, stream>>>(XP, z, gpart);
     finish_kernel<2><<<NQ2 / 256, 256, 0, stream>>>(gpart, invlam, D12, u, t);
     pz2_res_kernel<<<NQ2, 256, 0, stream>>>(XP, t, z, r, res);
-    lsolve_kernel<<<1, 1024, 0, stream>>>(M, Xinvs, res, y);
-    ltsolve_kernel<<<1, 1024, 0, stream>>>(M, Xinvs, y, dz);
+    lsolve_kernel<<<1, 1024, 0, stream>>>(P, Xinvs, res, y);
+    ltsolve_kernel<<<1, 1024, 0, stream>>>(P, Xinvs, y, dz);
     axpy_kernel<<<NQ2 / 256, 256, 0, stream>>>(z, dz);
   }
 
```

After: 2.539 ms. 1.05x faster.
